# Kernel tuning notes

Measured on AMD Instinct MI355X. Metric: run time of the kernel, lower is better.

## Reference

```python
import jax, jax.numpy as jnp
import numpy as np

D_MODEL = 1024
D_STATE = 16
D_CONV = 4
EXPAND = 2
D_INNER = D_MODEL * EXPAND          # 2048
DT_RANK = max(D_MODEL // 16, 1)     # 64
BATCH, SEQ_LEN = 2, 1024


def setup_inputs() -> dict:
    key = jax.random.key(0)
    ks = jax.random.split(key, 10)
    s = 0.02  # torch init std for linears
    x = jax.random.normal(ks[0], (BATCH, SEQ_LEN, D_MODEL), jnp.float32)
    W_in = jax.random.normal(ks[1], (2 * D_INNER, D_MODEL), jnp.float32) * s
    conv_w = jax.random.normal(ks[2], (D_INNER, 1, D_CONV), jnp.float32) * (1.0 / np.sqrt(D_CONV))
    conv_b = jnp.zeros((D_INNER,), jnp.float32)
    W_x = jax.random.normal(ks[3], (DT_RANK + 2 * D_STATE, D_INNER), jnp.float32) * s
    W_dt = jax.random.uniform(ks[4], (D_INNER, DT_RANK), jnp.float32,
                              -DT_RANK ** -0.5, DT_RANK ** -0.5)
    # dt bias init: inverse-softplus of dt ~ LogUniform(1e-3, 1e-1)
    dt = jnp.exp(jax.random.uniform(ks[5], (D_INNER,), jnp.float32)
                 * (np.log(0.1) - np.log(0.001)) + np.log(0.001))
    b_dt = dt + jnp.log(-jnp.expm1(-dt))
    A_log = jnp.log(jnp.tile(jnp.arange(1, D_STATE + 1, dtype=jnp.float32), (D_INNER, 1)))
    D_skip = jnp.ones((D_INNER,), jnp.float32)
    W_out = jax.random.normal(ks[6], (D_MODEL, D_INNER), jnp.float32) * s
    return {"x": x, "W_in": W_in, "conv_w": conv_w, "conv_b": conv_b, "W_x": W_x,
            "W_dt": W_dt, "b_dt": b_dt, "A_log": A_log, "D_skip": D_skip, "W_out": W_out}


def _causal_depthwise_conv(x_bld, conv_w, conv_b):
    # x_bld: [B, L, d_inner]; conv_w: [d_inner, 1, K]. Torch pads K-1 both
    # sides then slices [:seq_len] == causal left-pad of K-1.
    K = conv_w.shape[-1]
    lhs = jnp.pad(x_bld, ((0, 0), (K - 1, 0), (0, 0))).transpose(0, 2, 1)  # [B, C, L+K-1]
    out = jax.lax.conv_general_dilated(
        lhs, conv_w, window_strides=(1,), padding='VALID',
        dimension_numbers=('NCH', 'OIH', 'NCH'),
        feature_group_count=conv_w.shape[0])
    return out.transpose(0, 2, 1) + conv_b  # [B, L, d_inner]


def reference(x, W_in, conv_w, conv_b, W_x, W_dt, b_dt, A_log, D_skip, W_out):
    d_inner = W_in.shape[0] // 2
    dt_rank = W_dt.shape[1]
    d_state = A_log.shape[1]

    xz = jnp.einsum('bld,ed->ble', x, W_in)            # [B, L, 2*d_inner]
    x_ssm, z = xz[..., :d_inner], xz[..., d_inner:]
    x_ssm = jax.nn.silu(_causal_depthwise_conv(x_ssm, conv_w, conv_b))

    dbc = jnp.einsum('bld,ed->ble', x_ssm, W_x)        # [B, L, dt_rank+2*d_state]
    dt = jax.nn.softplus(jnp.einsum('blr,dr->bld', dbc[..., :dt_rank], W_dt) + b_dt)
    Bm = dbc[..., dt_rank:dt_rank + d_state]           # [B, L, d_state]
    Cm = dbc[..., dt_rank + d_state:]                  # [B, L, d_state]

    A = -jnp.exp(A_log)                                # [d_inner, d_state]
    A_bar = jnp.exp(dt[..., None] * A)                 # [B, L, d_inner, d_state]
    x_db = (x_ssm * dt)[..., None] * Bm[:, :, None, :] # [B, L, d_inner, d_state]

    def step(h, inp):
        a_t, xb_t, c_t = inp                           # [B,d,n], [B,d,n], [B,n]
        h = a_t * h + xb_t
        y_t = jnp.einsum('bn,bdn->bd', c_t, h)
        return h, y_t

    h0 = jnp.zeros((x.shape[0], d_inner, d_state), x.dtype)
    _, ys = jax.lax.scan(step, h0, (jnp.swapaxes(A_bar, 0, 1),
                                    jnp.swapaxes(x_db, 0, 1),
                                    jnp.swapaxes(Cm, 0, 1)))
    y = jnp.swapaxes(ys, 0, 1)                         # [B, L, d_inner]
    y = (y + x_ssm * D_skip) * jax.nn.silu(z)
    return jnp.einsum('bld,od->blo', y, W_out)         # [B, L, d_model]
```

## Files before the change

### kernel.cpp

```cpp
#include <hip/hip_runtime.h>
#include <hip/hip_bf16.h>
#include <math.h>

#define D_MODEL 1024
#define D_STATE 16
#define D_INNER 2048
#define DT_RANK 64
#define BATCH 2
#define SEQ_LEN 1024
#define T_TOTAL (BATCH * SEQ_LEN)

#define NC 64
#define CL 16

#define KS 16
#define KC 128
#define KT 64

typedef unsigned short u16;
typedef __bf16 bf16x8 __attribute__((ext_vector_type(8)));
typedef float f32x4 __attribute__((ext_vector_type(4)));

__device__ __forceinline__ u16 f2bf(float f) {
    unsigned u = __builtin_bit_cast(unsigned, f);
    u += 0x7FFFu + ((u >> 16) & 1u);
    return (u16)(u >> 16);
}

#define GLOAD_LDS16(g, l) \
    __builtin_amdgcn_global_load_lds((const __attribute__((address_space(1))) void*)(g), \
                                     (__attribute__((address_space(3))) void*)(l), 16, 0, 0)

__global__ __launch_bounds__(256) void cast_bf16_kernel(
    const float* __restrict__ in, u16* __restrict__ out)
{
    int i = blockIdx.x * 256 + threadIdx.x;
    float4 v = ((const float4*)in)[i];
    unsigned lo = (unsigned)f2bf(v.x) | ((unsigned)f2bf(v.y) << 16);
    unsigned hi = (unsigned)f2bf(v.z) | ((unsigned)f2bf(v.w) << 16);
    ((uint2*)out)[i] = make_uint2(lo, hi);
}

__global__ __launch_bounds__(256) void gemm_bf16_bt(
    const u16* __restrict__ A, int lda,
    const u16* __restrict__ Bw, int ldb,
    float* __restrict__ C, int ldc, int K)
{
    __shared__ u16 As[128][32];
    __shared__ u16 Bs[128][32];

    const int tid  = threadIdx.x;
    const int lane = tid & 63;
    const int wave = tid >> 6;
    const int wr   = wave >> 1;
    const int wc   = wave & 1;
    const int row0 = blockIdx.y * 128;
    const int col0 = blockIdx.x * 128;

    const int srow = tid >> 2;
    const int scol = (tid & 3) * 8;

    const u16* ag = A  + (size_t)(row0 + srow) * lda + scol;
    const u16* bg = Bw + (size_t)(col0 + srow) * ldb + scol;
    u16* asl = &As[0][0] + wave * 512;
    u16* bsl = &Bs[0][0] + wave * 512;

    f32x4 acc[4][4];
#pragma unroll
    for (int m = 0; m < 4; ++m)
#pragma unroll
        for (int n = 0; n < 4; ++n)
            acc[m][n] = (f32x4){0.f, 0.f, 0.f, 0.f};

    const int fr = lane & 15;
    const int kh = (lane >> 4) * 8;

    for (int k0 = 0; k0 < K; k0 += 32) {
        GLOAD_LDS16(ag + k0,                      asl);
        GLOAD_LDS16(ag + k0 + (size_t)64 * lda,   asl + 2048);
        GLOAD_LDS16(bg + k0,                      bsl);
        GLOAD_LDS16(bg + k0 + (size_t)64 * ldb,   bsl + 2048);
        __syncthreads();

        bf16x8 af[4], bf[4];
#pragma unroll
        for (int m = 0; m < 4; ++m)
            af[m] = *(const bf16x8*)&As[wr * 64 + m * 16 + fr][kh];
#pragma unroll
        for (int n = 0; n < 4; ++n)
            bf[n] = *(const bf16x8*)&Bs[wc * 64 + n * 16 + fr][kh];
#pragma unroll
        for (int m = 0; m < 4; ++m)
#pragma unroll
            for (int n = 0; n < 4; ++n)
                acc[m][n] = __builtin_amdgcn_mfma_f32_16x16x32_bf16(
                    af[m], bf[n], acc[m][n], 0, 0, 0);
        __syncthreads();
    }

    const int crow = (lane >> 4) * 4;
#pragma unroll
    for (int m = 0; m < 4; ++m) {
        const int gr = row0 + wr * 64 + m * 16 + crow;
#pragma unroll
        for (int n = 0; n < 4; ++n) {
            const int gc = col0 + wc * 64 + n * 16 + fr;
#pragma unroll
            for (int r = 0; r < 4; ++r)
                C[(size_t)(gr + r) * ldc + gc] = acc[m][n][r];
        }
    }
}

__global__ __launch_bounds__(256) void wx_partial(
    const float* __restrict__ A,
    const float* __restrict__ Bw,
    float* __restrict__ part)
{
    __shared__ float As[32][68];
    __shared__ float Bs[KT][98];

    const int tid = threadIdx.x;
    const int ks  = blockIdx.x;
    const int m0  = blockIdx.y * 32;
    const int k0  = ks * KC;

    const int tx = tid & 15;
    const int ty = tid >> 4;

    float acc[2][6] = {};

    for (int kk = 0; kk < KC; kk += KT) {
#pragma unroll
        for (int i = 0; i < 2; ++i) {
            int slot = tid + i * 256;
            int m  = slot >> 4;
            int kq = slot & 15;
            float4 v = *(const float4*)&A[(size_t)(m0 + m) * D_INNER + k0 + kk + kq * 4];
            *(float4*)&As[m][kq * 4] = v;
        }
#pragma unroll
        for (int i = 0; i < 6; ++i) {
            int slot = tid + i * 256;
            int n  = slot >> 4;
            int kq = slot & 15;
            float4 v = *(const float4*)&Bw[(size_t)n * D_INNER + k0 + kk + kq * 4];
            Bs[kq * 4 + 0][n] = v.x;
            Bs[kq * 4 + 1][n] = v.y;
            Bs[kq * 4 + 2][n] = v.z;
            Bs[kq * 4 + 3][n] = v.w;
        }
        __syncthreads();

#pragma unroll 8
        for (int k = 0; k < KT; ++k) {
            float a0 = As[ty * 2 + 0][k];
            float a1 = As[ty * 2 + 1][k];
            float2 b0 = *(const float2*)&Bs[k][tx * 6 + 0];
            float2 b1 = *(const float2*)&Bs[k][tx * 6 + 2];
            float2 b2 = *(const float2*)&Bs[k][tx * 6 + 4];
            float bv[6] = {b0.x, b0.y, b1.x, b1.y, b2.x, b2.y};
#pragma unroll
            for (int j = 0; j < 6; ++j) {
                acc[0][j] += a0 * bv[j];
                acc[1][j] += a1 * bv[j];
            }
        }
        __syncthreads();
    }

#pragma unroll
    for (int i = 0; i < 2; ++i) {
        size_t base = ((size_t)ks * T_TOTAL + (m0 + ty * 2 + i)) * 96 + tx * 6;
#pragma unroll
        for (int j = 0; j < 6; ++j)
            part[base + j] = acc[i][j];
    }
}

__global__ __launch_bounds__(256) void wx_reduce(
    const float* __restrict__ part, float* __restrict__ dbc)
{
    int i = blockIdx.x * 256 + threadIdx.x;
    float s = 0.f;
#pragma unroll
    for (int ks = 0; ks < KS; ++ks)
        s += part[(size_t)ks * T_TOTAL * 96 + i];
    dbc[i] = s;
}

__global__ __launch_bounds__(256) void dt_gemm(
    const float* __restrict__ A,
    const float* __restrict__ Bw,
    const float* __restrict__ bdt,
    float* __restrict__ dtb)
{
    __shared__ float As[16][65];
    __shared__ float Bs[16][65];

    const int tid = threadIdx.x;
    const int row0 = blockIdx.y * 64;
    const int col0 = blockIdx.x * 64;
    const int ty = tid >> 4;
    const int tx = tid & 15;

    float acc[4][4] = {};

    for (int k0 = 0; k0 < DT_RANK; k0 += 16) {
#pragma unroll
        for (int i = 0; i < 4; ++i) {
            int idx = tid + i * 256;
            int m = idx >> 4;
            int k = idx & 15;
            As[k][m] = A[(size_t)(row0 + m) * 96 + (k0 + k)];
        }
#pragma unroll
        for (int i = 0; i < 4; ++i) {
            int idx = tid + i * 256;
            int n = idx >> 4;
            int k = idx & 15;
            Bs[k][n] = Bw[(size_t)(col0 + n) * DT_RANK + (k0 + k)];
        }
        __syncthreads();

#pragma unroll
        for (int k = 0; k < 16; ++k) {
            float a[4], b[4];
#pragma unroll
            for (int i = 0; i < 4; ++i) a[i] = As[k][ty * 4 + i];
#pragma unroll
            for (int j = 0; j < 4; ++j) b[j] = Bs[k][tx * 4 + j];
#pragma unroll
            for (int i = 0; i < 4; ++i)
#pragma unroll
                for (int j = 0; j < 4; ++j)
                    acc[i][j] += a[i] * b[j];
        }
        __syncthreads();
    }

#pragma unroll
    for (int i = 0; i < 4; ++i) {
        int gm = row0 + ty * 4 + i;
#pragma unroll
        for (int j = 0; j < 4; ++j) {
            int gn = col0 + tx * 4 + j;
            float xv = acc[i][j] + bdt[gn];
            float sp = (xv > 20.f) ? xv : log1pf(__expf(xv));
            dtb[(size_t)gm * D_INNER + gn] = sp;
        }
    }
}

__global__ __launch_bounds__(256) void conv_silu_kernel(
    const float* __restrict__ xz,
    const float* __restrict__ cw,
    const float* __restrict__ cb,
    float* __restrict__ xc)
{
    int idx = blockIdx.x * 256 + threadIdx.x;
    int d = idx & (D_INNER - 1);
    int t = (idx >> 11) & (SEQ_LEN - 1);
    int b = idx >> 21;

    const float* base = xz + ((size_t)b * SEQ_LEN + t) * (2 * D_INNER) + d;
    float w0 = cw[d * 4 + 0], w1 = cw[d * 4 + 1], w2 = cw[d * 4 + 2], w3 = cw[d * 4 + 3];
    float acc = cb[d];
    if (t >= 3) acc += w0 * base[-3 * (2 * D_INNER)];
    if (t >= 2) acc += w1 * base[-2 * (2 * D_INNER)];
    if (t >= 1) acc += w2 * base[-1 * (2 * D_INNER)];
    acc += w3 * base[0];
    float s = acc / (1.f + __expf(-acc));
    xc[idx] = s;
}

__global__ __launch_bounds__(256) void scanA(
    const float* __restrict__ dbc,
    const float* __restrict__ dtv,
    const float* __restrict__ xc,
    const float* __restrict__ A_log,
    float* __restrict__ hbuf,
    float* __restrict__ sdt)
{
    __shared__ float sB[CL][16];

    const int tid = threadIdx.x;
    const int c = blockIdx.x;
    const int b = blockIdx.z;
    const int d = blockIdx.y * 256 + tid;
    const int t0 = c * CL;

    {
        int t = tid >> 4, e = tid & 15;
        sB[t][e] = dbc[(size_t)(b * SEQ_LEN + t0 + t) * 96 + DT_RANK + e];
    }

    float A[16];
#pragma unroll
    for (int i = 0; i < 4; ++i) {
        float4 v = *(const float4*)&A_log[d * 16 + i * 4];
        A[i * 4 + 0] = -__expf(v.x);
        A[i * 4 + 1] = -__expf(v.y);
        A[i * 4 + 2] = -__expf(v.z);
        A[i * 4 + 3] = -__expf(v.w);
    }
    __syncthreads();

    float h[16];
#pragma unroll
    for (int n = 0; n < 16; ++n) h[n] = 0.f;
    float sum = 0.f;

#pragma unroll 4
    for (int t = 0; t < CL; ++t) {
        size_t row = (size_t)(b * SEQ_LEN + t0 + t);
        float dtval = dtv[row * D_INNER + d];
        float xv    = xc [row * D_INNER + d];
        float w = xv * dtval;
        sum += dtval;
#pragma unroll
        for (int n = 0; n < 16; ++n) {
            float a = __expf(dtval * A[n]);
            h[n] = a * h[n] + w * sB[t][n];
        }
    }

    size_t o = (size_t)(b * NC + c) * 16 * D_INNER + d;
#pragma unroll
    for (int n = 0; n < 16; ++n)
        hbuf[o + (size_t)n * D_INNER] = h[n];
    sdt[(size_t)(b * NC + c) * D_INNER + d] = sum;
}

__global__ __launch_bounds__(256) void scanB(
    const float* __restrict__ A_log,
    const float* __restrict__ sdt,
    float* __restrict__ hbuf)
{
    int idx = blockIdx.x * 256 + threadIdx.x;
    int b  = idx >> 15;
    int nd = idx & 32767;
    int n  = nd >> 11;
    int d  = nd & (D_INNER - 1);

    const float A = -__expf(A_log[d * 16 + n]);
    float h = 0.f;
#pragma unroll 8
    for (int c = 0; c < NC; ++c) {
        size_t o = ((size_t)(b * NC + c) * 16 + n) * D_INNER + d;
        float tmp = hbuf[o];
        float P = __expf(A * sdt[(size_t)(b * NC + c) * D_INNER + d]);
        hbuf[o] = h;
        h = P * h + tmp;
    }
}

__global__ __launch_bounds__(256) void scanC(
    const float* __restrict__ dbc,
    const float* __restrict__ dtv,
    const float* __restrict__ xc,
    const float* __restrict__ xz,
    const float* __restrict__ A_log,
    const float* __restrict__ D_skip,
    const float* __restrict__ hbuf,
    u16* __restrict__ y)
{
    __shared__ float sB[CL][16];
    __shared__ float sC[CL][16];

    const int tid = threadIdx.x;
    const int c = blockIdx.x;
    const int b = blockIdx.z;
    const int d = blockIdx.y * 256 + tid;
    const int t0 = c * CL;

    {
        int t = tid >> 4, e = tid & 15;
        size_t row = (size_t)(b * SEQ_LEN + t0 + t);
        sB[t][e] = dbc[row * 96 + DT_RANK + e];
        sC[t][e] = dbc[row * 96 + DT_RANK + D_STATE + e];
    }

    float A[16];
#pragma unroll
    for (int i = 0; i < 4; ++i) {
        float4 v = *(const float4*)&A_log[d * 16 + i * 4];
        A[i * 4 + 0] = -__expf(v.x);
        A[i * 4 + 1] = -__expf(v.y);
        A[i * 4 + 2] = -__expf(v.z);
        A[i * 4 + 3] = -__expf(v.w);
    }
    const float Dv = D_skip[d];

    float h[16];
    size_t ho = (size_t)(b * NC + c) * 16 * D_INNER + d;
#pragma unroll
    for (int n = 0; n < 16; ++n)
        h[n] = hbuf[ho + (size_t)n * D_INNER];
    __syncthreads();

#pragma unroll 4
    for (int t = 0; t < CL; ++t) {
        size_t row = (size_t)(b * SEQ_LEN + t0 + t);
        float dtval = dtv[row * D_INNER + d];
        float xv    = xc [row * D_INNER + d];
        float zv    = xz [row * (2 * D_INNER) + D_INNER + d];
        float w = xv * dtval;
        float yv = 0.f;
#pragma unroll
        for (int n = 0; n < 16; ++n) {
            float a = __expf(dtval * A[n]);
            h[n] = a * h[n] + w * sB[t][n];
            yv += sC[t][n] * h[n];
        }
        float sig = 1.f / (1.f + __expf(-zv));
        y[row * D_INNER + d] = f2bf((yv + xv * Dv) * (zv * sig));
    }
}

extern "C" void kernel_launch(void* const* d_in, const int* in_sizes, int n_in,
                              void* d_out, int out_size, void* d_ws, size_t ws_size,
                              hipStream_t stream)
{
    const float* x      = (const float*)d_in[0];
    const float* W_in   = (const float*)d_in[1];
    const float* conv_w = (const float*)d_in[2];
    const float* conv_b = (const float*)d_in[3];
    const float* W_x    = (const float*)d_in[4];
    const float* W_dt   = (const float*)d_in[5];
    const float* b_dt   = (const float*)d_in[6];
    const float* A_log  = (const float*)d_in[7];
    const float* D_skip = (const float*)d_in[8];
    const float* W_out  = (const float*)d_in[9];
    float* out = (float*)d_out;

    float* ws = (float*)d_ws;
    float* xz    = ws;
    float* xc    = xz + (size_t)8388608;
    float* dbc   = xc + (size_t)4194304;
    float* dtbuf = dbc + (size_t)196608;
    float* hbuf  = dtbuf + (size_t)4194304;
    float* sdt   = hbuf + (size_t)4194304;
    u16* ybf = (u16*)(sdt + (size_t)262144);
    u16* xbf = ybf + (size_t)4194304;
    u16* wbf = xbf + (size_t)2097152;
    float* part = dtbuf;

    cast_bf16_kernel<<<2048, 256, 0, stream>>>(x, xbf);
    cast_bf16_kernel<<<4096, 256, 0, stream>>>(W_in, wbf);

    {
        dim3 grid(4096 / 128, 2048 / 128);
        gemm_bf16_bt<<<grid, 256, 0, stream>>>(xbf, D_MODEL, wbf, D_MODEL,
                                               xz, 2 * D_INNER, D_MODEL);
    }
    conv_silu_kernel<<<(T_TOTAL * D_INNER) / 256, 256, 0, stream>>>(xz, conv_w, conv_b, xc);

    {
        dim3 grid(KS, T_TOTAL / 32);
        wx_partial<<<grid, 256, 0, stream>>>(xc, W_x, part);
        wx_reduce<<<(T_TOTAL * 96) / 256, 256, 0, stream>>>(part, dbc);
    }
    {
        dim3 grid(D_INNER / 64, T_TOTAL / 64);
        dt_gemm<<<grid, 256, 0, stream>>>(dbc, W_dt, b_dt, dtbuf);
    }
    {
        dim3 gridA(NC, D_INNER / 256, BATCH);
        scanA<<<gridA, 256, 0, stream>>>(dbc, dtbuf, xc, A_log, hbuf, sdt);
        scanB<<<(BATCH * D_STATE * D_INNER) / 256, 256, 0, stream>>>(A_log, sdt, hbuf);
        scanC<<<gridA, 256, 0, stream>>>(dbc, dtbuf, xc, xz,
                                         A_log, D_skip, hbuf, ybf);
    }
    cast_bf16_kernel<<<2048, 256, 0, stream>>>(W_out, wbf);

    {
        dim3 grid(1024 / 128, 2048 / 128);
        gemm_bf16_bt<<<grid, 256, 0, stream>>>(ybf, D_INNER, wbf, D_INNER,
                                               out, D_MODEL, D_INNER);
    }
}
```

Before: 290.9 us.

## Use 8-wave GEMM blocks, split-K out-projection, and fuse input casts

Fuses the two fp32-to-bf16 casts for x and W_in into a single launch. The bf16 GEMM moves from 4 to 8 waves per 128x128 tile, each wave covering 64x32, with one load per thread per operand. The output projection now splits K into two halves over blockIdx.z, writing partial sums to scratch that a new reduce kernel adds together. The goal is more waves in flight and more blocks for the small 128-block output GEMM, at the cost of an extra reduction pass and additional global traffic.

After: 269.6 us. -7.3%, faster.

```diff
diff --git a/kernel.cpp b/kernel.cpp
--- a/kernel.cpp
+++ b/kernel.cpp
@@ -31,6 +31,19 @@
     __builtin_amdgcn_global_load_lds((const __attribute__((address_space(1))) void*)(g), \
                                      (__attribute__((address_space(3))) void*)(l), 16, 0, 0)
 
+__global__ __launch_bounds__(256) void cast2_bf16_kernel(
+    const float* __restrict__ in0, u16* __restrict__ out0, int nb0,
+    const float* __restrict__ in1, u16* __restrict__ out1)
+{
+    const float* in; u16* out; int i;
+    if (blockIdx.x < nb0) { in = in0; out = out0; i = blockIdx.x * 256 + threadIdx.x; }
+    else { in = in1; out = out1; i = (blockIdx.x - nb0) * 256 + threadIdx.x; }
+    float4 v = ((const float4*)in)[i];
+    unsigned lo = (unsigned)f2bf(v.x) | ((unsigned)f2bf(v.y) << 16);
+    unsigned hi = (unsigned)f2bf(v.z) | ((unsigned)f2bf(v.w) << 16);
+    ((uint2*)out)[i] = make_uint2(lo, hi);
+}
+
 __global__ __launch_bounds__(256) void cast_bf16_kernel(
     const float* __restrict__ in, u16* __restrict__ out)
 {
@@ -41,10 +54,10 @@
     ((uint2*)out)[i] = make_uint2(lo, hi);
 }
 
-__global__ __launch_bounds__(256) void gemm_bf16_bt(
+__global__ __launch_bounds__(512) void gemm_bf16_8w(
     const u16* __restrict__ A, int lda,
     const u16* __restrict__ Bw, int ldb,
-    float* __restrict__ C, int ldc, int K)
+    float* __restrict__ C, int ldc, int kchunk, size_t csize)
 {
     __shared__ u16 As[128][32];
     __shared__ u16 Bs[128][32];
@@ -52,10 +65,13 @@
     const int tid  = threadIdx.x;
     const int lane = tid & 63;
     const int wave = tid >> 6;
-    const int wr   = wave >> 1;
-    const int wc   = wave & 1;
+    const int wr   = wave >> 2;
+    const int wc   = wave & 3;
     const int row0 = blockIdx.y * 128;
     const int col0 = blockIdx.x * 128;
+    const int kbase = blockIdx.z * kchunk;
+
+    C += (size_t)blockIdx.z * csize;
 
     const int srow = tid >> 2;
     const int scol = (tid & 3) * 8;
@@ -65,34 +81,32 @@
     u16* asl = &As[0][0] + wave * 512;
     u16* bsl = &Bs[0][0] + wave * 512;
 
-    f32x4 acc[4][4];
+    f32x4 acc[4][2];
 #pragma unroll
     for (int m = 0; m < 4; ++m)
 #pragma unroll
-        for (int n = 0; n < 4; ++n)
+        for (int n = 0; n < 2; ++n)
             acc[m][n] = (f32x4){0.f, 0.f, 0.f, 0.f};
 
     const int fr = lane & 15;
     const int kh = (lane >> 4) * 8;
 
-    for (int k0 = 0; k0 < K; k0 += 32) {
-        GLOAD_LDS16(ag + k0,                      asl);
-        GLOAD_LDS16(ag + k0 + (size_t)64 * lda,   asl + 2048);
-        GLOAD_LDS16(bg + k0,                      bsl);
-        GLOAD_LDS16(bg + k0 + (size_t)64 * ldb,   bsl + 2048);
+    for (int k0 = kbase; k0 < kbase + kchunk; k0 += 32) {
+        GLOAD_LDS16(ag + k0, asl);
+        GLOAD_LDS16(bg + k0, bsl);
         __syncthreads();
 
-        bf16x8 af[4], bf[4];
+        bf16x8 af[4], bf[2];
 #pragma unroll
         for (int m = 0; m < 4; ++m)
             af[m] = *(const bf16x8*)&As[wr * 64 + m * 16 + fr][kh];
 #pragma unroll
-        for (int n = 0; n < 4; ++n)
-            bf[n] = *(const bf16x8*)&Bs[wc * 64 + n * 16 + fr][kh];
+        for (int n = 0; n < 2; ++n)
+            bf[n] = *(const bf16x8*)&Bs[wc * 32 + n * 16 + fr][kh];
 #pragma unroll
         for (int m = 0; m < 4; ++m)
 #pragma unroll
-            for (int n = 0; n < 4; ++n)
+            for (int n = 0; n < 2; ++n)
                 acc[m][n] = __builtin_amdgcn_mfma_f32_16x16x32_bf16(
                     af[m], bf[n], acc[m][n], 0, 0, 0);
         __syncthreads();
@@ -103,13 +117,22 @@
     for (int m = 0; m < 4; ++m) {
         const int gr = row0 + wr * 64 + m * 16 + crow;
 #pragma unroll
-        for (int n = 0; n < 4; ++n) {
-            const int gc = col0 + wc * 64 + n * 16 + fr;
+        for (int n = 0; n < 2; ++n) {
+            const int gc = col0 + wc * 32 + n * 16 + fr;
 #pragma unroll
             for (int r = 0; r < 4; ++r)
                 C[(size_t)(gr + r) * ldc + gc] = acc[m][n][r];
         }
     }
+}
+
+__global__ __launch_bounds__(256) void reduce2_kernel(
+    const float* __restrict__ part, float* __restrict__ out, size_t n4)
+{
+    size_t i = (size_t)blockIdx.x * 256 + threadIdx.x;
+    float4 a = ((const float4*)part)[i];
+    float4 b = ((const float4*)part)[i + n4];
+    ((float4*)out)[i] = make_float4(a.x + b.x, a.y + b.y, a.z + b.z, a.w + b.w);
 }
 
 __global__ __launch_bounds__(256) void wx_partial(
@@ -445,14 +468,14 @@
     u16* xbf = ybf + (size_t)4194304;
     u16* wbf = xbf + (size_t)2097152;
     float* part = dtbuf;
-
-    cast_bf16_kernel<<<2048, 256, 0, stream>>>(x, xbf);
-    cast_bf16_kernel<<<4096, 256, 0, stream>>>(W_in, wbf);
-
-    {
-        dim3 grid(4096 / 128, 2048 / 128);
-        gemm_bf16_bt<<<grid, 256, 0, stream>>>(xbf, D_MODEL, wbf, D_MODEL,
-                                               xz, 2 * D_INNER, D_MODEL);
+    float* part7 = hbuf;
+
+    cast2_bf16_kernel<<<6144, 256, 0, stream>>>(x, xbf, 2048, W_in, wbf);
+
+    {
+        dim3 grid(4096 / 128, 2048 / 128, 1);
+        gemm_bf16_8w<<<grid, 512, 0, stream>>>(xbf, D_MODEL, wbf, D_MODEL,
+                                               xz, 2 * D_INNER, D_MODEL, 0);
     }
     conv_silu_kernel<<<(T_TOTAL * D_INNER) / 256, 256, 0, stream>>>(xz, conv_w, conv_b, xc);
 
@@ -475,8 +498,11 @@
     cast_bf16_kernel<<<2048, 256, 0, stream>>>(W_out, wbf);
 
     {
-        dim3 grid(1024 / 128, 2048 / 128);
-        gemm_bf16_bt<<<grid, 256, 0, stream>>>(ybf, D_INNER, wbf, D_INNER,
-                                               out, D_MODEL, D_INNER);
-    }
-}
+        dim3 grid(1024 / 128, 2048 / 128, 2);
+        gemm_bf16_8w<<<grid, 512, 0, stream>>>(ybf, D_INNER, wbf, D_INNER,
+                                               part7, D_MODEL, 1024,
+                                               (size_t)T_TOTAL * D_MODEL);
+        reduce2_kernel<<<(T_TOTAL * D_MODEL / 4) / 256, 256, 0, stream>>>(
+            part7, out, (size_t)T_TOTAL * D_MODEL / 4);
+    }
+}
```
